# Performance work log

Hardware: AMD Instinct MI355X
Metric: run time of the kernel (lower is better)

## Reference

```python
import jax, jax.numpy as jnp
import numpy as np

EPS = 1e-5

def _inorm(t):
    # InstanceNorm2d, affine=False: normalize each (B,C) plane over H,W
    m = t.mean((2, 3), keepdims=True)
    v = t.var((2, 3), keepdims=True)
    return (t - m) * jax.lax.rsqrt(v + EPS)

def _conv(x, w, b):
    y = jax.lax.conv_general_dilated(x, w, (1, 1), 'SAME',
        dimension_numbers=('NCHW', 'OIHW', 'NCHW'))
    return y + b[None, :, None, None]

def _ss2d(xh, in_proj_w, conv_w, conv_b, x_proj_w, dt_w, dt_b, A_logs, Ds,
          out_norm_g, out_norm_b, out_proj_w):
    # xh: (B,H,W,C) -> (B,H,W,C). VMamba-style 4-direction selective scan.
    B, H, W, C = xh.shape
    Di = in_proj_w.shape[0] // 2
    n = A_logs.shape[-1]
    R = dt_w.shape[-1]
    L = H * W
    xz = xh @ in_proj_w.T                      # (B,H,W,2*Di)
    xin, z = xz[..., :Di], xz[..., Di:]
    xc = xin.transpose(0, 3, 1, 2)             # (B,Di,H,W)
    xc = jax.lax.conv_general_dilated(xc, conv_w, (1, 1), 'SAME',
        feature_group_count=Di, dimension_numbers=('NCHW', 'OIHW', 'NCHW'))
    xc = jax.nn.silu(xc + conv_b[None, :, None, None])
    x1 = xc.reshape(B, Di, L)                  # row-major scan
    x2 = xc.transpose(0, 1, 3, 2).reshape(B, Di, L)  # col-major scan
    xs = jnp.stack([x1, x2, x1[..., ::-1], x2[..., ::-1]], axis=1)  # (B,4,Di,L)
    x_dbl = jnp.einsum('bkdl,kcd->bkcl', xs, x_proj_w)
    dts = jnp.einsum('bkrl,kdr->bkdl', x_dbl[:, :, :R], dt_w)
    Bs, Cs = x_dbl[:, :, R:R + n], x_dbl[:, :, R + n:]
    delta = jax.nn.softplus(dts + dt_b[None, :, :, None])
    A = -jnp.exp(A_logs)                       # (4,Di,n)
    scan_in = (jnp.moveaxis(xs, -1, 0), jnp.moveaxis(delta, -1, 0),
               jnp.moveaxis(Bs, -1, 0), jnp.moveaxis(Cs, -1, 0))
    def step(h, inp):
        u, d, b, c = inp                       # u,d:(B,4,Di)  b,c:(B,4,n)
        h = jnp.exp(d[..., None] * A) * h + (d * u)[..., None] * b[:, :, None, :]
        return h, (h * c[:, :, None, :]).sum(-1)
    h0 = jnp.zeros((B, 4, Di, n), xh.dtype)
    _, ys = jax.lax.scan(step, h0, scan_in)    # ys: (L,B,4,Di)
    out_y = jnp.moveaxis(ys, 0, -1) + Ds[None, :, :, None] * xs  # (B,4,Di,L)
    def _wh(t):
        return t.reshape(B, Di, W, H).transpose(0, 1, 3, 2).reshape(B, Di, L)
    y = out_y[:, 0] + out_y[:, 2, :, ::-1] + _wh(out_y[:, 1]) + _wh(out_y[:, 3, :, ::-1])
    y = y.transpose(0, 2, 1).reshape(B, H, W, Di)
    mu = y.mean(-1, keepdims=True)
    v = y.var(-1, keepdims=True)
    y = (y - mu) * jax.lax.rsqrt(v + EPS) * out_norm_g + out_norm_b
    return (y * jax.nn.silu(z)) @ out_proj_w.T

def setup_inputs():
    key = jax.random.key(0)
    ks = jax.random.split(key, 16)
    B, C, H, W = 4, 96, 64, 64
    Di, n, R, K, SQ, CC = 192, 8, 6, 4, 16, 16
    f = jnp.float32
    nrm = lambda k, s: 0.02 * jax.random.normal(k, s, dtype=f)
    inp = {}
    inp['x'] = jax.random.normal(ks[0], (B, C, H, W), dtype=f)
    inp['dz'] = jax.random.uniform(ks[1], (B, 1, H, W), dtype=f)
    inp['in_proj_w'] = nrm(ks[2], (2 * Di, C))
    inp['conv_w'] = nrm(ks[3], (Di, 1, 3, 3))
    inp['conv_b'] = jnp.zeros((Di,), f)
    inp['x_proj_w'] = nrm(ks[4], (K, R + 2 * n, Di))
    inp['dt_w'] = nrm(ks[5], (K, Di, R))
    inp['dt_b'] = 0.01 * jnp.ones((K, Di), f)
    inp['A_logs'] = jnp.log(jnp.tile(jnp.arange(1, n + 1, dtype=f)[None, None, :], (K, Di, 1)))
    inp['Ds'] = jnp.ones((K, Di), f)
    inp['out_norm_g'] = jnp.ones((Di,), f)
    inp['out_norm_b'] = jnp.zeros((Di,), f)
    inp['out_proj_w'] = nrm(ks[6], (C, Di))
    inp['ln_g'] = jnp.ones((C,), f)
    inp['ln_b'] = jnp.zeros((C,), f)
    inp['skip_ss2d'] = jnp.ones((C,), f)
    inp['cca_w1'] = nrm(ks[7], (SQ, C))
    inp['cca_b1'] = jnp.zeros((SQ,), f)
    inp['cca_w2'] = nrm(ks[8], (C, SQ))
    inp['cca_b2'] = jnp.zeros((C,), f)
    inp['bnc_w1'] = nrm(ks[9], (CC, C, 1, 1))
    inp['bnc_b1'] = jnp.zeros((CC,), f)
    inp['bnc_w2'] = nrm(ks[10], (CC, CC, 3, 3))
    inp['bnc_b2'] = jnp.zeros((CC,), f)
    inp['bnc_w3'] = nrm(ks[11], (C, CC, 1, 1))
    inp['bnc_b3'] = jnp.zeros((C,), f)
    return inp

def reference(x, dz, in_proj_w, conv_w, conv_b, x_proj_w, dt_w, dt_b, A_logs, Ds,
              out_norm_g, out_norm_b, out_proj_w, ln_g, ln_b, skip_ss2d,
              cca_w1, cca_b1, cca_w2, cca_b2,
              bnc_w1, bnc_b1, bnc_w2, bnc_b2, bnc_w3, bnc_b3):
    SKIP_CCA, SKIP_BNC = 0.4, 1.0
    # 1) channel cross-attention block (dz-guided SE), residual w/ skip 0.4
    xn = _inorm(x)
    pooled = (xn * dz).sum((2, 3)) / (dz.sum((2, 3)) + 1e-6)  # (B,C)
    s = jax.nn.sigmoid(jax.nn.relu(pooled @ cca_w1.T + cca_b1) @ cca_w2.T + cca_b2)
    x = xn * s[:, :, None, None] + SKIP_CCA * x
    # 2) SS2D block in NHWC, residual w/ learned per-channel skip weight
    xh = x.transpose(0, 2, 3, 1)
    mu = xh.mean(-1, keepdims=True)
    v = xh.var(-1, keepdims=True)
    xln = (xh - mu) * jax.lax.rsqrt(v + EPS) * ln_g + ln_b
    y = _ss2d(xln, in_proj_w, conv_w, conv_b, x_proj_w, dt_w, dt_b, A_logs, Ds,
              out_norm_g, out_norm_b, out_proj_w)
    x = (y + skip_ss2d * xh).transpose(0, 3, 1, 2)
    # 3) bottleneck conv block, residual w/ skip 1.0
    xn = _inorm(x)
    h = jax.nn.relu(_conv(xn, bnc_w1, bnc_b1))
    h = jax.nn.relu(_conv(h, bnc_w2, bnc_b2))
    h = _conv(h, bnc_w3, bnc_b3)
    return h + SKIP_BNC * x
```

## Files before the change

### kernel.cpp

```cpp
#include <hip/hip_runtime.h>
#include <hip/hip_bf16.h>
#include <math.h>

constexpr int TOT_IN = 1685008;

constexpr size_t F_x    = 64;
constexpr size_t F_dz   = F_x + 1572864;
constexpr size_t F_ipw  = F_dz + 16384;
constexpr size_t F_convw= F_ipw + 36864;
constexpr size_t F_convb= F_convw + 1728;
constexpr size_t F_xpw  = F_convb + 192;
constexpr size_t F_dtw  = F_xpw + 16896;
constexpr size_t F_dtb  = F_dtw + 4608;
constexpr size_t F_alog = F_dtb + 768;
constexpr size_t F_Dsv  = F_alog + 6144;
constexpr size_t F_ong  = F_Dsv + 768;
constexpr size_t F_onb  = F_ong + 192;
constexpr size_t F_opw  = F_onb + 192;
constexpr size_t F_lng  = F_opw + 18432;
constexpr size_t F_lnb  = F_lng + 96;
constexpr size_t F_skip = F_lnb + 96;
constexpr size_t F_cw1  = F_skip + 96;
constexpr size_t F_cb1  = F_cw1 + 1536;
constexpr size_t F_cw2  = F_cb1 + 16;
constexpr size_t F_cb2  = F_cw2 + 1536;
constexpr size_t F_bw1  = F_cb2 + 96;
constexpr size_t F_bb1  = F_bw1 + 1536;
constexpr size_t F_bw2  = F_bb1 + 16;
constexpr size_t F_bb2  = F_bw2 + 2304;
constexpr size_t F_bw3  = F_bb2 + 16;
constexpr size_t F_bb3  = F_bw3 + 1536;
constexpr size_t F_stat = 1685504;
constexpr size_t F_mean1= F_stat;
constexpr size_t F_rstd1= F_stat + 384;
constexpr size_t F_wsum = F_stat + 768;
constexpr size_t F_sca  = F_stat + 1216;
constexpr size_t F_mean2= F_stat + 1664;
constexpr size_t F_rstd2= F_stat + 2048;
constexpr size_t F_xcca = 1689600;
constexpr size_t F_xln  = F_xcca + 1572864;
constexpr size_t F_xin  = F_xln  + 1572864;
constexpr size_t F_z    = F_xin  + 3145728;
constexpr size_t F_xct  = F_z    + 3145728;
constexpr size_t F_xdbl = F_xct  + 3145728;
constexpr size_t F_old1 = F_xdbl + 1572864;
constexpr size_t F_xccaT= F_old1 + 3145728;
constexpr size_t F_yc   = F_xccaT+ 1572864;
constexpr size_t F_tb   = F_yc   + 3145728;
constexpr size_t F_x2   = F_tb   + 3145728;
constexpr size_t F_h1   = F_x2   + 1572864;
constexpr size_t F_h2   = F_h1   + 262144;
constexpr size_t F_xpwt = F_h2   + 262144;
constexpr size_t F_ipwt = F_xpwt + 18432;
constexpr size_t F_opwt = F_ipwt + 36864;
constexpr size_t F_cwt  = F_opwt + 18432;
constexpr size_t F_hend = F_xin;
constexpr size_t F_apr  = F_tb;
constexpr size_t F_hcar = F_old1;

__constant__ int y4off[16] = {
  3262464, 4048896, 4835328, 5621760, 6408192, 7194624,
  18991104, 19777536,
  20563968, 21350400, 22136832, 22923264,
  23709696, 24496128, 25282560, 26068992};

__constant__ int g_off[27] = {
  0,1572864,1589248,1626112,1627840,1628032,1644928,1649536,1650304,1656448,
  1657216,1657408,1657600,1676032,1676128,1676224,1676320,1677856,1677872,1679408,
  1679504,1681040,1681056,1683360,1683376,1684912,1685008};

struct Ptrs26 { const void* p[26]; };

static __device__ __forceinline__ float sigmoidf_(float x){ return 1.f/(1.f+__expf(-x)); }
static __device__ __forceinline__ float siluf_(float x){ return x*sigmoidf_(x); }
static __device__ __forceinline__ float softplusf_(float x){ return x>15.f ? x : log1pf(__expf(x)); }
static __device__ __forceinline__ int mapk_(int k,int l){
  switch(k){
    case 0: return l;
    case 1: return ((l&63)<<6)|(l>>6);
    case 2: return 4095-l;
    default:{ int l2=4095-l; return ((l2&63)<<6)|(l2>>6); }
  }
}

__global__ void k_convert(Ptrs26 ps, float* __restrict__ F){
  int bf = (((const unsigned int*)ps.p[9])[0] == 0x3F803F80u) ? 1 : 0;
  int stride = gridDim.x*blockDim.x;
  for (int idx = blockIdx.x*blockDim.x+threadIdx.x; idx < TOT_IN; idx += stride){
    int lo = 0, hi = 26;
    while (hi - lo > 1){ int mid = (lo+hi)>>1; if (idx >= g_off[mid]) lo = mid; else hi = mid; }
    int s = lo;
    int loc = idx - g_off[s];
    float v;
    if (bf) v = __bfloat162float(((const __hip_bfloat16*)ps.p[s])[loc]);
    else    v = ((const float*)ps.p[s])[loc];
    F[64 + idx] = v;
  }
}

__global__ void k_wtrans(float* __restrict__ F){
  int idx = blockIdx.x*256 + threadIdx.x;
  if (idx < 18432){
    int c = idx % 24; int d = (idx/24) % 192; int k = idx/(24*192);
    F[F_xpwt + idx] = (c < 22) ? F[F_xpw + (size_t)(k*22 + c)*192 + d] : 0.f;
  } else if (idx < 18432 + 36864){
    int i = idx - 18432;
    int j = i % 384, c = i / 384;
    F[F_ipwt + i] = F[F_ipw + (size_t)j*96 + c];
  } else if (idx < 18432 + 36864 + 18432){
    int i = idx - 18432 - 36864;
    int c = i % 96, d = i / 96;
    F[F_opwt + i] = F[F_opw + (size_t)c*192 + d];
  } else if (idx < 18432 + 36864 + 18432 + 1728){
    int i = idx - 18432 - 36864 - 18432;
    int d = i % 192, tap = i / 192;
    F[F_cwt + i] = F[F_convw + (size_t)d*9 + tap];
  }
}

__global__ void k_inorm1(float* __restrict__ F){
  int bc = blockIdx.x; int b = bc/96;
  const float* xp  = F + F_x  + (size_t)bc*4096;
  const float* dzp = F + F_dz + (size_t)b*4096;
  float s=0.f, s2=0.f, sw=0.f;
  for (int l=threadIdx.x; l<4096; l+=256){ float v=xp[l]; s+=v; s2+=v*v; sw+=v*dzp[l]; }
  for (int m=32;m;m>>=1){ s+=__shfl_xor(s,m); s2+=__shfl_xor(s2,m); sw+=__shfl_xor(sw,m); }
  __shared__ float red[12];
  int wid = threadIdx.x>>6;
  if ((threadIdx.x&63)==0){ red[wid]=s; red[4+wid]=s2; red[8+wid]=sw; }
  __syncthreads();
  if (threadIdx.x==0){
    s = red[0]+red[1]+red[2]+red[3];
    s2= red[4]+red[5]+red[6]+red[7];
    sw= red[8]+red[9]+red[10]+red[11];
    float mean = s*(1.f/4096.f);
    float var  = s2*(1.f/4096.f) - mean*mean;
    F[F_mean1+bc]=mean; F[F_rstd1+bc]=rsqrtf(var+1e-5f); F[F_wsum+bc]=sw;
  }
}

__global__ void k_cca(float* __restrict__ F){
  __shared__ float ps[96], hid[16], red[2];
  int b = blockIdx.x, t = threadIdx.x;
  const float* dzp = F + F_dz + (size_t)b*4096;
  float s=0.f;
  for (int l=t; l<4096; l+=128) s += dzp[l];
  for (int m=32;m;m>>=1) s += __shfl_xor(s,m);
  if ((t&63)==0) red[t>>6] = s;
  __syncthreads();
  float dzs = red[0]+red[1];
  if (t<96){
    int bc = b*96+t;
    ps[t] = F[F_rstd1+bc]*(F[F_wsum+bc]-F[F_mean1+bc]*dzs)/(dzs+1e-6f);
  }
  __syncthreads();
  if (t<16){
    float a = F[F_cb1+t];
    for (int c=0;c<96;c++) a += ps[c]*F[F_cw1+t*96+c];
    hid[t] = fmaxf(a,0.f);
  }
  __syncthreads();
  if (t<96){
    float a = F[F_cb2+t];
    for (int j=0;j<16;j++) a += hid[j]*F[F_cw2+t*16+j];
    F[F_sca+b*96+t] = sigmoidf_(a);
  }
}

__global__ __launch_bounds__(256) void k_ccat(float* __restrict__ F){
  __shared__ float T[96*33];
  int b = blockIdx.x >> 7; int l0 = (blockIdx.x & 127)*32;
  for (int i = threadIdx.x; i < 3072; i += 256){
    int l = i & 31, c = i >> 5;
    int bc = b*96 + c;
    float v = F[F_x + (size_t)bc*4096 + l0 + l];
    float xv = (v - F[F_mean1+bc])*F[F_rstd1+bc]*F[F_sca+bc] + 0.4f*v;
    F[F_xcca + (size_t)bc*4096 + l0 + l] = xv;
    T[c*33 + l] = xv;
  }
  __syncthreads();
  for (int i = threadIdx.x; i < 3072; i += 256){
    int c = i % 96, l = i / 96;
    F[F_xccaT + ((size_t)(b*4096 + l0 + l))*96 + c] = T[c*33 + l];
  }
}

__global__ __launch_bounds__(128) void k_gemm1(
    const float* __restrict__ xt, const float* __restrict__ lng,
    const float* __restrict__ lnb, const float* __restrict__ wt1,
    float* __restrict__ xin, float* __restrict__ z)
{
  int lb = blockIdx.x & 127; int jc = blockIdx.x >> 7;
  int t = lb*128 + threadIdx.x;
  const float4* rp = (const float4*)(xt + (size_t)t*96);
  float s=0.f, s2=0.f;
  for (int c4=0; c4<24; c4++){
    float4 v = rp[c4];
    s  += v.x+v.y+v.z+v.w;
    s2 += v.x*v.x+v.y*v.y+v.z*v.z+v.w*v.w;
  }
  float mean = s*(1.f/96.f);
  float rstd = rsqrtf(s2*(1.f/96.f) - mean*mean + 1e-5f);
  const float4* gp = (const float4*)lng;
  const float4* bp = (const float4*)lnb;
  const float* wbase = wt1 + jc*24;
  float acc[24];
  #pragma unroll
  for (int j=0;j<24;j++) acc[j]=0.f;
  for (int c4=0; c4<24; c4++){
    float4 av = rp[c4]; float4 g = gp[c4]; float4 bb = bp[c4];
    float tv[4];
    tv[0] = (av.x-mean)*rstd*g.x + bb.x;
    tv[1] = (av.y-mean)*rstd*g.y + bb.y;
    tv[2] = (av.z-mean)*rstd*g.z + bb.z;
    tv[3] = (av.w-mean)*rstd*g.w + bb.w;
    #pragma unroll
    for (int cc=0; cc<4; cc++){
      const float* wr = wbase + (size_t)(c4*4+cc)*384;
      #pragma unroll
      for (int j=0;j<24;j++) acc[j] += tv[cc] * wr[j];
    }
  }
  float* op = (jc < 8) ? (xin + (size_t)t*192 + jc*24)
                       : (z   + (size_t)t*192 + (jc-8)*24);
  float4* o4 = (float4*)op;
  #pragma unroll
  for (int q=0;q<6;q++) o4[q] = make_float4(acc[q*4],acc[q*4+1],acc[q*4+2],acc[q*4+3]);
}

__global__ void k_dwconv(const float* __restrict__ xin, const float* __restrict__ cwt,
                         const float* __restrict__ cb, float* __restrict__ xct){
  int idx = blockIdx.x*256 + threadIdx.x;
  if (idx >= 786432) return;
  int d4 = idx % 48; int bl = idx / 48; int l = bl & 4095; int b = bl >> 12;
  int h = l >> 6, w = l & 63;
  const float4* xp = (const float4*)(xin + (size_t)b*4096*192);
  const float4* wp = (const float4*)cwt;
  float4 bias = ((const float4*)cb)[d4];
  float ax=bias.x, ay=bias.y, az=bias.z, aw=bias.w;
  #pragma unroll
  for (int ky=0; ky<3; ky++){
    int hh = h + ky - 1; if ((unsigned)hh > 63u) continue;
    #pragma unroll
    for (int kx=0; kx<3; kx++){
      int ww = w + kx - 1; if ((unsigned)ww > 63u) continue;
      float4 xv = xp[(size_t)(hh*64+ww)*48 + d4];
      float4 wv = wp[(ky*3+kx)*48 + d4];
      ax += xv.x*wv.x; ay += xv.y*wv.y; az += xv.z*wv.z; aw += xv.w*wv.w;
    }
  }
  float4 o;
  o.x = ax*sigmoidf_(ax); o.y = ay*sigmoidf_(ay);
  o.z = az*sigmoidf_(az); o.w = aw*sigmoidf_(aw);
  ((float4*)xct)[idx] = o;
}

__global__ __launch_bounds__(256) void k_xdbl(
    const float* __restrict__ xct, const float* __restrict__ wt,
    float* __restrict__ xdbl)
{
  int lb = blockIdx.x & 15; int bk = blockIdx.x >> 4;
  int b = bk >> 2, k = bk & 3;
  int l = lb*256 + threadIdx.x;
  int sp = mapk_(k, l);
  const float4* rp = (const float4*)(xct + ((size_t)b*4096 + sp)*192);
  const float* wk = wt + (size_t)k*192*24;
  float acc[24];
  #pragma unroll
  for (int c=0;c<24;c++) acc[c]=0.f;
  #pragma unroll 2
  for (int d4=0; d4<48; d4++){
    float4 av = rp[d4];
    #pragma unroll
    for (int j=0;j<4;j++){
      float ad = (j==0)?av.x:(j==1)?av.y:(j==2)?av.z:av.w;
      const float* wd = wk + (d4*4+j)*24;
      #pragma unroll
      for (int c=0;c<22;c++) acc[c] += ad * wd[c];
    }
  }
  acc[22]=0.f; acc[23]=0.f;
  float4* op = (float4*)(xdbl + ((size_t)bk*4096 + l)*24);
  #pragma unroll
  for (int q=0;q<6;q++) op[q] = make_float4(acc[q*4],acc[q*4+1],acc[q*4+2],acc[q*4+3]);
}

__global__ __launch_bounds__(192) void k_scan1(
    const float* __restrict__ xdbl, const float* __restrict__ xct,
    const float* __restrict__ alogs, const float* __restrict__ dtws,
    const float* __restrict__ dtbs,
    float* __restrict__ hend, float* __restrict__ apr)
{
  int chunk = blockIdx.x & 127; int bk = blockIdx.x >> 7;
  int b = bk >> 2, k = bk & 3; int d = threadIdx.x;
  const float* alog = alogs + (size_t)(k*192+d)*8;
  float A_[8], hh[8], ap[8];
  #pragma unroll
  for (int i=0;i<8;i++){ A_[i] = -__expf(alog[i]); hh[i]=0.f; ap[i]=1.f; }
  bool structured = fabsf(A_[0] + 1.f) < 1e-4f;
  #pragma unroll
  for (int i=1;i<8;i++) structured = structured && (fabsf(A_[i] - (float)(i+1)*A_[0]) <= 1e-4f*fabsf(A_[i]));
  float dtw_[6];
  #pragma unroll
  for (int r=0;r<6;r++) dtw_[r] = dtws[(size_t)(k*192+d)*6 + r];
  float dtb_ = dtbs[k*192 + d];
  const float* xB = xdbl + ((size_t)bk*4096 + chunk*32)*24;
  const float* xc = xct + (size_t)b*4096*192 + d;
  if (structured){
    #pragma unroll 4
    for (int s=0;s<32;s++){
      const float* xl = xB + s*24;
      float dt = dtb_;
      #pragma unroll
      for (int r=0;r<6;r++) dt += xl[r]*dtw_[r];
      int sp = mapk_(k, chunk*32+s);
      float u = xc[(size_t)sp*192];
      float t = __expf(dt);
      float a1 = __builtin_amdgcn_rcpf(1.f + t);
      float delta = (dt > 15.f) ? dt : __logf(1.f + t);
      float du = delta*u;
      float a = a1;
      #pragma unroll
      for (int i=0;i<8;i++){
        hh[i] = a*hh[i] + du*xl[6+i];
        ap[i] *= a;
        a *= a1;
      }
    }
  } else {
    for (int s=0;s<32;s++){
      const float* xl = xB + s*24;
      float dt = dtb_;
      #pragma unroll
      for (int r=0;r<6;r++) dt += xl[r]*dtw_[r];
      int sp = mapk_(k, chunk*32+s);
      float u = xc[(size_t)sp*192];
      float delta = softplusf_(dt);
      float du = delta*u;
      #pragma unroll
      for (int i=0;i<8;i++){
        float a = __expf(delta*A_[i]);
        hh[i] = a*hh[i] + du*xl[6+i];
        ap[i] *= a;
      }
    }
  }
  size_t base = ((size_t)(bk<<7) + chunk)*1536 + d*8;
  #pragma unroll
  for (int i=0;i<8;i++){ hend[base+i]=hh[i]; apr[base+i]=ap[i]; }
}

__global__ void k_carry(const float* __restrict__ hend, const float* __restrict__ apr,
                        float* __restrict__ hcar){
  int t = blockIdx.x*256 + threadIdx.x;
  if (t >= 16*1536) return;
  int di8 = t % 1536; int bk = t / 1536;
  float carry = 0.f;
  for (int c=0;c<128;c++){
    size_t idx = ((size_t)(bk<<7) + c)*1536 + di8;
    hcar[idx] = carry;
    carry = apr[idx]*carry + hend[idx];
  }
}

__global__ __launch_bounds__(192) void k_scan2(
    const float* __restrict__ xdbl, const float* __restrict__ xct,
    const float* __restrict__ alogs, const float* __restrict__ dtws,
    const float* __restrict__ dtbs, const float* __restrict__ Dsv,
    const float* __restrict__ hcar, float* __restrict__ yout)
{
  int chunk = blockIdx.x & 127; int bk = blockIdx.x >> 7;
  int b = bk >> 2, k = bk & 3; int d = threadIdx.x;
  const float* alog = alogs + (size_t)(k*192+d)*8;
  float A_[8], hh[8];
  size_t cb = ((size_t)(bk<<7) + chunk)*1536 + d*8;
  #pragma unroll
  for (int i=0;i<8;i++){ A_[i] = -__expf(alog[i]); hh[i] = hcar[cb+i]; }
  bool structured = fabsf(A_[0] + 1.f) < 1e-4f;
  #pragma unroll
  for (int i=1;i<8;i++) structured = structured && (fabsf(A_[i] - (float)(i+1)*A_[0]) <= 1e-4f*fabsf(A_[i]));
  float dtw_[6];
  #pragma unroll
  for (int r=0;r<6;r++) dtw_[r] = dtws[(size_t)(k*192+d)*6 + r];
  float dtb_ = dtbs[k*192 + d];
  float Dsc  = Dsv[k*192 + d];
  const float* xB = xdbl + ((size_t)bk*4096 + chunk*32)*24;
  const float* xc = xct + (size_t)b*4096*192 + d;
  float* yo = yout + (size_t)y4off[bk] + ((size_t)(chunk*32))*192 + d;
  if (structured){
    #pragma unroll 4
    for (int s=0;s<32;s++){
      const float* xl = xB + s*24;
      float dt = dtb_;
      #pragma unroll
      for (int r=0;r<6;r++) dt += xl[r]*dtw_[r];
      int sp = mapk_(k, chunk*32+s);
      float u = xc[(size_t)sp*192];
      float t = __expf(dt);
      float a1 = __builtin_amdgcn_rcpf(1.f + t);
      float delta = (dt > 15.f) ? dt : __logf(1.f + t);
      float du = delta*u;
      float a = a1, y = 0.f;
      #pragma unroll
      for (int i=0;i<8;i++){
        hh[i] = a*hh[i] + du*xl[6+i];
        y += hh[i]*xl[14+i];
        a *= a1;
      }
      yo[(size_t)s*192] = y + Dsc*u;
    }
  } else {
    for (int s=0;s<32;s++){
      const float* xl = xB + s*24;
      float dt = dtb_;
      #pragma unroll
      for (int r=0;r<6;r++) dt += xl[r]*dtw_[r];
      int sp = mapk_(k, chunk*32+s);
      float u = xc[(size_t)sp*192];
      float delta = softplusf_(dt);
      float du = delta*u;
      float y = 0.f;
      #pragma unroll
      for (int i=0;i<8;i++){
        float a = __expf(delta*A_[i]);
        hh[i] = a*hh[i] + du*xl[6+i];
        y += hh[i]*xl[14+i];
      }
      yo[(size_t)s*192] = y + Dsc*u;
    }
  }
}

__global__ void k_tnorm(float* __restrict__ F){
  int wid = threadIdx.x >> 6, lane = threadIdx.x & 63;
  int p = blockIdx.x*4 + wid;
  int b = p >> 12, sp = p & 4095;
  int l1 = ((sp&63)<<6)|(sp>>6);
  const float* y0 = F + (size_t)y4off[b*4+0] + (size_t)sp*192;
  const float* y1 = F + (size_t)y4off[b*4+1] + (size_t)l1*192;
  const float* y2 = F + (size_t)y4off[b*4+2] + (size_t)(4095-sp)*192;
  const float* y3 = F + (size_t)y4off[b*4+3] + (size_t)(4095-l1)*192;
  float v[3]; float s=0.f, s2=0.f;
  #pragma unroll
  for (int j=0;j<3;j++){
    int dd = j*64+lane;
    v[j] = y0[dd] + y1[dd] + y2[dd] + y3[dd];
    s += v[j]; s2 += v[j]*v[j];
  }
  for (int m=32;m;m>>=1){ s+=__shfl_xor(s,m); s2+=__shfl_xor(s2,m); }
  float mean = s*(1.f/192.f);
  float rstd = rsqrtf(s2*(1.f/192.f) - mean*mean + 1e-5f);
  size_t base = (size_t)p*192;
  #pragma unroll
  for (int j=0;j<3;j++){
    int dd = j*64+lane;
    float zv = F[F_z + base + dd];
    float t = (v[j]-mean)*rstd*F[F_ong+dd] + F[F_onb+dd];
    F[F_xct + base + dd] = t * siluf_(zv);
  }
}

__global__ __launch_bounds__(128) void k_gemm2(
    const float* __restrict__ tb, const float* __restrict__ wt2,
    const float* __restrict__ skip, const float* __restrict__ xcca,
    float* __restrict__ x2)
{
  int lb = blockIdx.x & 127; int cbk = blockIdx.x >> 7;
  int t = lb*128 + threadIdx.x;
  int b = t >> 12, l = t & 4095;
  const float4* rp = (const float4*)(tb + (size_t)t*192);
  const float* wbase = wt2 + cbk*12;
  float acc[12];
  #pragma unroll
  for (int c=0;c<12;c++) acc[c]=0.f;
  #pragma unroll 2
  for (int d4=0; d4<48; d4++){
    float4 av = rp[d4];
    #pragma unroll
    for (int dd=0; dd<4; dd++){
      float ad = (dd==0)?av.x:(dd==1)?av.y:(dd==2)?av.z:av.w;
      const float* wr = wbase + (size_t)(d4*4+dd)*96;
      #pragma unroll
      for (int c=0;c<12;c++) acc[c] += ad * wr[c];
    }
  }
  #pragma unroll
  for (int c=0;c<12;c++){
    int cg = cbk*12 + c;
    size_t o = ((size_t)(b*96+cg))*4096 + l;
    x2[o] = acc[c] + skip[cg]*xcca[o];
  }
}

__global__ void k_inorm2(float* __restrict__ F){
  int bc = blockIdx.x;
  const float* xp = F + F_x2 + (size_t)bc*4096;
  float s=0.f, s2=0.f;
  for (int l=threadIdx.x; l<4096; l+=256){ float v=xp[l]; s+=v; s2+=v*v; }
  for (int m=32;m;m>>=1){ s+=__shfl_xor(s,m); s2+=__shfl_xor(s2,m); }
  __shared__ float red[8];
  int wid = threadIdx.x>>6;
  if ((threadIdx.x&63)==0){ red[wid]=s; red[4+wid]=s2; }
  __syncthreads();
  if (threadIdx.x==0){
    s = red[0]+red[1]+red[2]+red[3];
    s2= red[4]+red[5]+red[6]+red[7];
    float mean = s*(1.f/4096.f);
    float var  = s2*(1.f/4096.f) - mean*mean;
    F[F_mean2+bc]=mean; F[F_rstd2+bc]=rsqrtf(var+1e-5f);
  }
}

__global__ void k_bnc1(float* __restrict__ F){
  int idx = blockIdx.x*256 + threadIdx.x;
  if (idx >= 4*16*4096) return;
  int l = idx & 4095; int bj = idx >> 12; int j = bj % 16; int b = bj / 16;
  float acc = F[F_bb1 + j];
  const float* wp = F + F_bw1 + j*96;
  for (int c=0;c<96;c++){
    int bc = b*96+c;
    float xn = (F[F_x2 + (size_t)bc*4096 + l] - F[F_mean2+bc])*F[F_rstd2+bc];
    acc += xn*wp[c];
  }
  F[F_h1+idx] = fmaxf(acc, 0.f);
}

__global__ void k_bnc2(float* __restrict__ F){
  int idx = blockIdx.x*256 + threadIdx.x;
  if (idx >= 4*16*4096) return;
  int l = idx & 4095; int bj = idx >> 12; int j = bj % 16; int b = bj / 16;
  int h = l >> 6, w = l & 63;
  float acc = F[F_bb2 + j];
  const float* h1p = F + F_h1 + (size_t)b*16*4096;
  const float* wp  = F + F_bw2 + j*16*9;
  for (int jp=0; jp<16; jp++){
    #pragma unroll
    for (int ky=0; ky<3; ky++){
      int hh = h + ky - 1; if (hh < 0 || hh > 63) continue;
      #pragma unroll
      for (int kx=0; kx<3; kx++){
        int ww = w + kx - 1; if (ww < 0 || ww > 63) continue;
        acc += h1p[(size_t)jp*4096 + hh*64+ww] * wp[jp*9 + ky*3 + kx];
      }
    }
  }
  F[F_h2+idx] = fmaxf(acc, 0.f);
}

__global__ void k_bnc3(float* __restrict__ F, void* __restrict__ out, const unsigned int* __restrict__ ds){
  int idx = blockIdx.x*256 + threadIdx.x;
  if (idx >= 1572864) return;
  int l = idx & 4095; int bc = idx >> 12; int c = bc % 96; int b = bc / 96;
  float acc = F[F_bb3 + c];
  const float* h2p = F + F_h2 + (size_t)b*16*4096 + l;
  const float* wp  = F + F_bw3 + c*16;
  #pragma unroll
  for (int j=0;j<16;j++) acc += h2p[(size_t)j*4096]*wp[j];
  float res = acc + F[F_x2+idx];
  if (ds[0]==0x3F803F80u) ((__hip_bfloat16*)out)[idx] = __float2bfloat16(res);
  else                    ((float*)out)[idx] = res;
}

extern "C" void kernel_launch(void* const* d_in, const int* in_sizes, int n_in,
                              void* d_out, int out_size, void* d_ws, size_t ws_size,
                              hipStream_t stream) {
  (void)in_sizes; (void)n_in; (void)out_size; (void)ws_size;
  float* F = (float*)d_ws;

  Ptrs26 ps;
  for (int i=0;i<26;i++) ps.p[i] = d_in[i];

  k_convert<<<2048, 256, 0, stream>>>(ps, F);
  k_wtrans<<<296, 256, 0, stream>>>(F);

  k_inorm1<<<384, 256, 0, stream>>>(F);
  k_cca   <<<4,   128, 0, stream>>>(F);
  k_ccat  <<<512, 256, 0, stream>>>(F);
  k_gemm1 <<<2048,128, 0, stream>>>(F+F_xccaT, F+F_lng, F+F_lnb, F+F_ipwt, F+F_xin, F+F_z);
  k_dwconv<<<3072,256, 0, stream>>>(F+F_xin, F+F_cwt, F+F_convb, F+F_xct);
  k_xdbl  <<<256, 256, 0, stream>>>(F+F_xct, F+F_xpwt, F+F_xdbl);
  k_scan1 <<<2048,192, 0, stream>>>(F+F_xdbl, F+F_xct, F+F_alog, F+F_dtw, F+F_dtb,
                                    F+F_hend, F+F_apr);
  k_carry <<<96,  256, 0, stream>>>(F+F_hend, F+F_apr, F+F_hcar);
  k_scan2 <<<2048,192, 0, stream>>>(F+F_xdbl, F+F_xct, F+F_alog, F+F_dtw, F+F_dtb,
                                    F+F_Dsv, F+F_hcar, F);
  k_tnorm <<<4096,256, 0, stream>>>(F);
  k_gemm2 <<<1024,128, 0, stream>>>(F+F_xct, F+F_opwt, F+F_skip, F+F_xcca, F+F_x2);
  k_inorm2<<<384, 256, 0, stream>>>(F);
  k_bnc1  <<<1024,256, 0, stream>>>(F);
  k_bnc2  <<<1024,256, 0, stream>>>(F);
  k_bnc3  <<<6144,256, 0, stream>>>(F, d_out, (const unsigned int*)d_in[9]);
}
```

Measured before the change: 379.4 us.

## Move LayerNorm into transpose kernel and tile in_proj GEMM through shared memory

LayerNorm over channels now runs once per token inside the transpose kernel, using a shuffle reduction, and the normalized NHWC tensor is written out directly. The in_proj GEMM is rewritten as a 64x64 shared-memory tiled kernel with a 4x4 register micro-tile per thread. The old version recomputed the LN statistics in each of 16 column blocks and read weights from global memory per thread. The new layout aims for data reuse and fewer redundant global loads, at the cost of more shared memory per block (about 52KB), which may limit occupancy.

```diff
diff --git a/kernel.cpp b/kernel.cpp
--- a/kernel.cpp
+++ b/kernel.cpp
@@ -169,6 +169,7 @@
 
 __global__ __launch_bounds__(256) void k_ccat(float* __restrict__ F){
   __shared__ float T[96*33];
+  __shared__ float mns[32], rss[32];
   int b = blockIdx.x >> 7; int l0 = (blockIdx.x & 127)*32;
   for (int i = threadIdx.x; i < 3072; i += 256){
     int l = i & 31, c = i >> 5;
@@ -179,53 +180,63 @@
     T[c*33 + l] = xv;
   }
   __syncthreads();
+  {
+    int l = threadIdx.x >> 3, p = threadIdx.x & 7;
+    float s=0.f, s2=0.f;
+    for (int c=p; c<96; c+=8){ float v = T[c*33 + l]; s+=v; s2+=v*v; }
+    for (int m=4;m;m>>=1){ s += __shfl_xor(s,m); s2 += __shfl_xor(s2,m); }
+    if (p==0){
+      float mean = s*(1.f/96.f);
+      mns[l] = mean;
+      rss[l] = rsqrtf(s2*(1.f/96.f) - mean*mean + 1e-5f);
+    }
+  }
+  __syncthreads();
   for (int i = threadIdx.x; i < 3072; i += 256){
     int c = i % 96, l = i / 96;
-    F[F_xccaT + ((size_t)(b*4096 + l0 + l))*96 + c] = T[c*33 + l];
-  }
-}
-
-__global__ __launch_bounds__(128) void k_gemm1(
-    const float* __restrict__ xt, const float* __restrict__ lng,
-    const float* __restrict__ lnb, const float* __restrict__ wt1,
+    float xv = T[c*33 + l];
+    F[F_xccaT + ((size_t)(b*4096 + l0 + l))*96 + c] =
+        (xv - mns[l])*rss[l]*F[F_lng+c] + F[F_lnb+c];
+  }
+}
+
+__global__ __launch_bounds__(256) void k_gemm1(
+    const float* __restrict__ xln, const float* __restrict__ wt1,
     float* __restrict__ xin, float* __restrict__ z)
 {
-  int lb = blockIdx.x & 127; int jc = blockIdx.x >> 7;
-  int t = lb*128 + threadIdx.x;
-  const float4* rp = (const float4*)(xt + (size_t)t*96);
-  float s=0.f, s2=0.f;
-  for (int c4=0; c4<24; c4++){
-    float4 v = rp[c4];
-    s  += v.x+v.y+v.z+v.w;
-    s2 += v.x*v.x+v.y*v.y+v.z*v.z+v.w*v.w;
-  }
-  float mean = s*(1.f/96.f);
-  float rstd = rsqrtf(s2*(1.f/96.f) - mean*mean + 1e-5f);
-  const float4* gp = (const float4*)lng;
-  const float4* bp = (const float4*)lnb;
-  const float* wbase = wt1 + jc*24;
-  float acc[24];
-  #pragma unroll
-  for (int j=0;j<24;j++) acc[j]=0.f;
-  for (int c4=0; c4<24; c4++){
-    float4 av = rp[c4]; float4 g = gp[c4]; float4 bb = bp[c4];
-    float tv[4];
-    tv[0] = (av.x-mean)*rstd*g.x + bb.x;
-    tv[1] = (av.y-mean)*rstd*g.y + bb.y;
-    tv[2] = (av.z-mean)*rstd*g.z + bb.z;
-    tv[3] = (av.w-mean)*rstd*g.w + bb.w;
+  __shared__ float As[96*68];
+  __shared__ float Ws[96*68];
+  int lt = blockIdx.x & 255, jb = blockIdx.x >> 8;
+  int l0 = lt*64, j0 = jb*64;
+  for (int i = threadIdx.x; i < 6144; i += 256){
+    int li = i / 96, c = i - (i/96)*96;
+    As[c*68 + li] = xln[((size_t)(l0+li))*96 + c];
+  }
+  for (int i = threadIdx.x; i < 6144; i += 256){
+    int c = i >> 6, jj = i & 63;
+    Ws[c*68 + jj] = wt1[(size_t)c*384 + j0 + jj];
+  }
+  __syncthreads();
+  int li0 = (threadIdx.x & 15)*4, jj0 = (threadIdx.x >> 4)*4;
+  float acc[4][4] = {};
+  #pragma unroll 4
+  for (int c = 0; c < 96; c++){
+    float4 a = *(const float4*)(As + c*68 + li0);
+    float4 w = *(const float4*)(Ws + c*68 + jj0);
+    float ar[4] = {a.x, a.y, a.z, a.w};
+    float wr[4] = {w.x, w.y, w.z, w.w};
     #pragma unroll
-    for (int cc=0; cc<4; cc++){
-      const float* wr = wbase + (size_t)(c4*4+cc)*384;
-      #pragma unroll
-      for (int j=0;j<24;j++) acc[j] += tv[cc] * wr[j];
-    }
-  }
-  float* op = (jc < 8) ? (xin + (size_t)t*192 + jc*24)
-                       : (z   + (size_t)t*192 + (jc-8)*24);
-  float4* o4 = (float4*)op;
-  #pragma unroll
-  for (int q=0;q<6;q++) o4[q] = make_float4(acc[q*4],acc[q*4+1],acc[q*4+2],acc[q*4+3]);
+    for (int r=0;r<4;r++)
+      #pragma unroll
+      for (int q=0;q<4;q++) acc[r][q] += ar[r]*wr[q];
+  }
+  float* base = (j0 < 192) ? xin : z;
+  int joff = (j0 < 192) ? (j0 + jj0) : (j0 - 192 + jj0);
+  #pragma unroll
+  for (int r=0;r<4;r++){
+    *(float4*)&base[(size_t)(l0+li0+r)*192 + joff] =
+        make_float4(acc[r][0], acc[r][1], acc[r][2], acc[r][3]);
+  }
 }
 
 __global__ void k_dwconv(const float* __restrict__ xin, const float* __restrict__ cwt,
@@ -576,7 +587,7 @@
   k_inorm1<<<384, 256, 0, stream>>>(F);
   k_cca   <<<4,   128, 0, stream>>>(F);
   k_ccat  <<<512, 256, 0, stream>>>(F);
-  k_gemm1 <<<2048,128, 0, stream>>>(F+F_xccaT, F+F_lng, F+F_lnb, F+F_ipwt, F+F_xin, F+F_z);
+  k_gemm1 <<<1536,256, 0, stream>>>(F+F_xccaT, F+F_ipwt, F+F_xin, F+F_z);
   k_dwconv<<<3072,256, 0, stream>>>(F+F_xin, F+F_cwt, F+F_convb, F+F_xct);
   k_xdbl  <<<256, 256, 0, stream>>>(F+F_xct, F+F_xpwt, F+F_xdbl);
   k_scan1 <<<2048,192, 0, stream>>>(F+F_xdbl, F+F_xct, F+F_alog, F+F_dtw, F+F_dtb,
```

New measurement: 368.6 us. 1.03x faster.
